# Performance work log

Measured on AMD Instinct MI355X. Metric: run time of the kernel, lower is better.

The kernel has to match this reference:

```python
import jax, jax.numpy as jnp
import numpy as np

HIDDEN = 256
N_PROT = 12288
N_MOL = 6144
N_BATCH = 32


def setup_inputs() -> dict:
    key = jax.random.key(0)
    ks = jax.random.split(key, 10)
    s = 1.0 / np.sqrt(HIDDEN)  # torch Linear default init scale
    inp = {
        "prot_embed": jax.random.normal(ks[0], (N_PROT, HIDDEN), jnp.float32),
        "mol_embed": jax.random.normal(ks[1], (N_MOL, HIDDEN), jnp.float32),
        "prot_batch": jnp.sort(jax.random.randint(ks[2], (N_PROT,), 0, N_BATCH)),
        "mol_batch": jnp.sort(jax.random.randint(ks[3], (N_MOL,), 0, N_BATCH)),
        "Wq": jax.random.uniform(ks[4], (HIDDEN, HIDDEN), jnp.float32, -s, s),
        "bq": jax.random.uniform(ks[5], (HIDDEN,), jnp.float32, -s, s),
        "Wk": jax.random.uniform(ks[6], (HIDDEN, HIDDEN), jnp.float32, -s, s),
        "bk": jax.random.uniform(ks[7], (HIDDEN,), jnp.float32, -s, s),
        "Wv": jax.random.uniform(ks[8], (HIDDEN, HIDDEN), jnp.float32, -s, s),
        "bv": jax.random.uniform(ks[9], (HIDDEN,), jnp.float32, -s, s),
    }
    return inp


def reference(prot_embed, mol_embed, prot_batch, mol_batch, Wq, bq, Wk, bk, Wv, bv):
    # Linear projections (torch nn.Linear: x @ W.T + b)
    Q = prot_embed @ Wq.T + bq            # [N, H]
    K = mol_embed @ Wk.T + bk             # [M, H]
    V = mol_embed @ Wv.T + bv             # [M, H]

    scale = 1.0 / jnp.sqrt(jnp.asarray(Q.shape[-1], Q.dtype))
    scores = (Q @ K.T) * scale            # [N, M]

    # block mask: same-batch pairs only
    mask = prot_batch[:, None] == mol_batch[None, :]   # [N, M] bool
    neg_inf = jnp.asarray(-jnp.inf, scores.dtype)
    scores = jnp.where(mask, scores, neg_inf)

    # stable masked softmax; rows with no valid key -> all zeros
    # (matches torch softmax(-inf row) -> nan -> nan_to_num(0.0))
    row_any = mask.any(axis=-1, keepdims=True)
    mx = jnp.max(scores, axis=-1, keepdims=True)
    mx = jnp.where(row_any, mx, 0.0)
    e = jnp.exp(scores - mx)              # exp(-inf)=0 on masked entries
    denom = jnp.sum(e, axis=-1, keepdims=True)
    attn = e / jnp.where(row_any, denom, 1.0)  # [N, M]

    out = attn @ V                        # [N, H]
    return out, attn
```

## Files before the change

### kernel.cpp

```cpp
#include <hip/hip_runtime.h>

#define NPROT 12288
#define NMOL  6144
#define HID   256
#define NB    32

#define WQ_O   4718592
#define WK_O   4784128
#define WV_O   4849664
#define BQ_O   4915200
#define BK_O   4915456
#define BV_O   4915712
#define Q_O    4915968
#define K_O    8061696
#define VT_O   9634560
#define END_O  11207424

typedef __attribute__((ext_vector_type(4))) float f32x4;
typedef __attribute__((ext_vector_type(8))) short bf16x8;
typedef unsigned short u16;
typedef unsigned int   u32;

__device__ __forceinline__ float b2f(u16 u){
  union { u32 i; float f; } v; v.i = ((u32)u) << 16; return v.f;
}
__device__ __forceinline__ u16 f2b(float f){
  union { float fl; u32 i; } v; v.fl = f;
  u32 i = v.i;
  return (u16)((i + 0x7FFFu + ((i >> 16) & 1u)) >> 16);
}

__global__ __launch_bounds__(256) void prep_kernel(
    const float* __restrict__ Wq, const float* __restrict__ Wk,
    const float* __restrict__ Wv, const float* __restrict__ bq,
    const float* __restrict__ bk, const float* __restrict__ bv,
    const int* __restrict__ pb, const int* __restrict__ mb,
    int* __restrict__ rg, u16* __restrict__ cvt)
{
  int g = blockIdx.x * 256 + threadIdx.x;
  const float* src = nullptr; u16* dst = nullptr; int off = 0;
  if      (g < 16384) { src = Wq; dst = cvt + WQ_O; off = g; }
  else if (g < 32768) { src = Wk; dst = cvt + WK_O; off = g - 16384; }
  else if (g < 49152) { src = Wv; dst = cvt + WV_O; off = g - 32768; }
  else if (g < 49216) { src = bq; dst = cvt + BQ_O; off = g - 49152; }
  else if (g < 49280) { src = bk; dst = cvt + BK_O; off = g - 49216; }
  else if (g < 49344) { src = bv; dst = cvt + BV_O; off = g - 49280; }
  if (src){
    f32x4 v = *(const f32x4*)(src + (size_t)off * 4);
    ushort4 o;
    o.x = f2b(v[0]); o.y = f2b(v[1]); o.z = f2b(v[2]); o.w = f2b(v[3]);
    *(ushort4*)(dst + (size_t)off * 4) = o;
  }

  if (blockIdx.x == 0 && threadIdx.x < 64){
    int t = threadIdx.x;
    const int* arr = (t < 32) ? pb : mb;
    int n          = (t < 32) ? NPROT : NMOL;
    int target     = (t & 31) + 1;
    int lo = 0, hi = n;
    while (lo < hi){
      int mid = (lo + hi) >> 1;
      if (arr[mid] < target) lo = mid + 1; else hi = mid;
    }
    int end = lo;
    int prev = __shfl(end, t - 1);
    int start = ((t & 31) == 0) ? 0 : prev;
    int b = t & 31;
    if (t < 32){ rg[b] = start; rg[32 + b] = end; }
    else       { rg[64 + b] = start; rg[96 + b] = end; }
  }
}

__global__ __launch_bounds__(256) void proj_kernel(
    const float* __restrict__ prot, const float* __restrict__ mol,
    const u16* __restrict__ cvt,
    u16* __restrict__ Q, u16* __restrict__ K, u16* __restrict__ Vt)
{
  __shared__ u16 xlds[16][264];
  __shared__ u16 tlds[4][64][18];
  int rb = blockIdx.x;
  int proj;
  const float* X; const u16 *W, *B;
  if      (rb < 768) { proj = 0; X = prot; W = cvt + WQ_O; B = cvt + BQ_O; }
  else if (rb < 1152){ proj = 1; rb -= 768;  X = mol; W = cvt + WK_O; B = cvt + BK_O; }
  else               { proj = 2; rb -= 1152; X = mol; W = cvt + WV_O; B = cvt + BV_O; }
  int rowbase = rb * 16;

  {
    int r  = threadIdx.x >> 4;
    int c0 = (threadIdx.x & 15) * 16;
    const float* xp = X + (size_t)(rowbase + r) * HID + c0;
    f32x4 v0 = *(const f32x4*)(xp);
    f32x4 v1 = *(const f32x4*)(xp + 4);
    f32x4 v2 = *(const f32x4*)(xp + 8);
    f32x4 v3 = *(const f32x4*)(xp + 12);
    u16* d = &xlds[r][c0];
    ushort4 o0, o1, o2, o3;
    o0.x = f2b(v0[0]); o0.y = f2b(v0[1]); o0.z = f2b(v0[2]); o0.w = f2b(v0[3]);
    o1.x = f2b(v1[0]); o1.y = f2b(v1[1]); o1.z = f2b(v1[2]); o1.w = f2b(v1[3]);
    o2.x = f2b(v2[0]); o2.y = f2b(v2[1]); o2.z = f2b(v2[2]); o2.w = f2b(v2[3]);
    o3.x = f2b(v3[0]); o3.y = f2b(v3[1]); o3.z = f2b(v3[2]); o3.w = f2b(v3[3]);
    *(ushort4*)(d)      = o0;
    *(ushort4*)(d + 4)  = o1;
    *(ushort4*)(d + 8)  = o2;
    *(ushort4*)(d + 12) = o3;
  }
  __syncthreads();

  int wave = threadIdx.x >> 6, lane = threadIdx.x & 63;
  int m = lane & 15, q = lane >> 4;
  int colbase = wave * 64;

  f32x4 acc[4] = {};
  for (int k0 = 0; k0 < HID; k0 += 32){
    bf16x8 a = *(const bf16x8*)(&xlds[m][k0 + q*8]);
    #pragma unroll
    for (int ct = 0; ct < 4; ct++){
      bf16x8 b = *(const bf16x8*)(W + (size_t)(colbase + ct*16 + m) * HID + k0 + q*8);
      acc[ct] = __builtin_amdgcn_mfma_f32_16x16x32_bf16(a, b, acc[ct], 0, 0, 0);
    }
  }

  if (proj < 2){
    u16* O = (proj == 0) ? Q : K;
    #pragma unroll
    for (int ct = 0; ct < 4; ct++){
      int col = colbase + ct*16 + m;
      float bb = b2f(B[col]);
      #pragma unroll
      for (int r = 0; r < 4; r++){
        int row = rowbase + q*4 + r;
        O[(size_t)row * HID + col] = f2b(acc[ct][r] + bb);
      }
    }
  } else {
    #pragma unroll
    for (int ct = 0; ct < 4; ct++){
      int lc = ct*16 + m;
      float bb = b2f(B[colbase + lc]);
      #pragma unroll
      for (int r = 0; r < 4; r++)
        tlds[wave][lc][q*4 + r] = f2b(acc[ct][r] + bb);
    }
    __syncthreads();
    int col = colbase + lane;
    u32 packed[8];
    #pragma unroll
    for (int i = 0; i < 8; i++){
      u16 lo = tlds[wave][lane][2*i];
      u16 hi = tlds[wave][lane][2*i+1];
      packed[i] = (u32)lo | ((u32)hi << 16);
    }
    u16* dst = Vt + (size_t)col * NMOL + rowbase;
    uint4 v0 = {packed[0], packed[1], packed[2], packed[3]};
    uint4 v1 = {packed[4], packed[5], packed[6], packed[7]};
    *(uint4*)dst = v0;
    *(uint4*)(dst + 8) = v1;
  }
}

__global__ __launch_bounds__(256) void attn_kernel(
    const int* __restrict__ rg,
    const u16* __restrict__ Q, const u16* __restrict__ K,
    const u16* __restrict__ Vt, float* __restrict__ dout)
{
  __shared__ u16 P[16][392];
  __shared__ float mxw[4][16];
  __shared__ float smw[4][16];
  const float scale = 0.0625f;
  float* outf  = dout;
  float* attnf = dout + (size_t)NPROT * HID;

  int b = blockIdx.y;
  int ps = rg[b], pe = rg[32+b], ms = rg[64+b], me = rg[96+b];
  int Np = pe - ps, Nm = me - ms;
  if (Np <= 0) return;

  int wave = threadIdx.x >> 6, lane = threadIdx.x & 63;
  int m = lane & 15, q = lane >> 4;
  int ntiles = (Np + 15) >> 4;

  int bs = 0, ce = 0;
  if (Nm > 0){ bs = ms & ~31; ce = bs + ((me - bs + 31) & ~31); }

  for (int tile = blockIdx.x; tile < ntiles; tile += 32){
    int row0 = ps + tile * 16;
    int qr = min(row0 + m, NPROT - 1);
    const u16* qrow = Q + (size_t)qr * HID;
    bf16x8 qf[8];
    #pragma unroll
    for (int kk = 0; kk < 8; kk++)
      qf[kk] = *(const bf16x8*)(qrow + kk*32 + q*8);

    if (Nm > 0){
      int myj0 = bs + wave * 16;
      f32x4 sreg[6];
      float mx[4] = {-1e30f, -1e30f, -1e30f, -1e30f};
      #pragma unroll
      for (int c = 0; c < 6; c++){
        int j0 = myj0 + 64*c;
        if (j0 < ce){
          int col = j0 + m;
          bool valid = (col >= ms) && (col < me);
          const u16* krow = K + (size_t)col * HID;
          f32x4 s0 = {0.f,0.f,0.f,0.f}, s1 = {0.f,0.f,0.f,0.f};
          #pragma unroll
          for (int kk = 0; kk < 4; kk++){
            bf16x8 kb0 = *(const bf16x8*)(krow + kk*32 + q*8);
            bf16x8 kb1 = *(const bf16x8*)(krow + (kk+4)*32 + q*8);
            s0 = __builtin_amdgcn_mfma_f32_16x16x32_bf16(qf[kk],   kb0, s0, 0, 0, 0);
            s1 = __builtin_amdgcn_mfma_f32_16x16x32_bf16(qf[kk+4], kb1, s1, 0, 0, 0);
          }
          f32x4 sv;
          #pragma unroll
          for (int r = 0; r < 4; r++)
            sv[r] = valid ? (s0[r] + s1[r]) * scale : -1e30f;
          sreg[c] = sv;
          float cm[4];
          #pragma unroll
          for (int r = 0; r < 4; r++) cm[r] = sv[r];
          #pragma unroll
          for (int d = 1; d < 16; d <<= 1)
            #pragma unroll
            for (int r = 0; r < 4; r++)
              cm[r] = fmaxf(cm[r], __shfl_xor(cm[r], d, 16));
          #pragma unroll
          for (int r = 0; r < 4; r++) mx[r] = fmaxf(mx[r], cm[r]);
        }
      }
      if (m == 0){
        #pragma unroll
        for (int r = 0; r < 4; r++) mxw[wave][q*4 + r] = mx[r];
      }
      __syncthreads();
      float gmx[4];
      #pragma unroll
      for (int r = 0; r < 4; r++){
        int row = q*4 + r;
        float M = mxw[0][row];
        #pragma unroll
        for (int w = 1; w < 4; w++) M = fmaxf(M, mxw[w][row]);
        gmx[r] = M;
      }

      float sm[4] = {0.f, 0.f, 0.f, 0.f};
      #pragma unroll
      for (int c = 0; c < 6; c++){
        int j0 = myj0 + 64*c;
        if (j0 < ce){
          f32x4 e;
          #pragma unroll
          for (int r = 0; r < 4; r++) e[r] = __expf(sreg[c][r] - gmx[r]);
          sreg[c] = e;
          float t[4];
          #pragma unroll
          for (int r = 0; r < 4; r++) t[r] = e[r];
          #pragma unroll
          for (int d = 1; d < 16; d <<= 1)
            #pragma unroll
            for (int r = 0; r < 4; r++)
              t[r] += __shfl_xor(t[r], d, 16);
          #pragma unroll
          for (int r = 0; r < 4; r++) sm[r] += t[r];
        }
      }
      if (m == 0){
        #pragma unroll
        for (int r = 0; r < 4; r++) smw[wave][q*4 + r] = sm[r];
      }
      __syncthreads();
      float ginv[4];
      #pragma unroll
      for (int r = 0; r < 4; r++){
        int row = q*4 + r;
        float S = smw[0][row] + smw[1][row] + smw[2][row] + smw[3][row];
        ginv[r] = (S > 0.f) ? (1.f / S) : 0.f;
      }

      #pragma unroll
      for (int c = 0; c < 6; c++){
        int j0 = myj0 + 64*c;
        if (j0 < ce){
          int col = j0 + m;
          int jl = j0 - bs;
          bool valid = (col >= ms) && (col < me);
          #pragma unroll
          for (int r = 0; r < 4; r++){
            float p = sreg[c][r] * ginv[r];
            P[q*4 + r][jl + m] = f2b(p);
            int row = row0 + q*4 + r;
            if (valid && row < pe)
              __builtin_nontemporal_store(p, attnf + (size_t)row * NMOL + col);
          }
        }
      }
      __syncthreads();

      f32x4 oacc[4] = {};
      for (int j0 = bs; j0 < ce; j0 += 32){
        int jl = j0 - bs;
        bf16x8 a = *(const bf16x8*)(&P[m][jl + q*8]);
        #pragma unroll
        for (int c2 = 0; c2 < 4; c2++){
          int ct = wave*4 + c2;
          bf16x8 vb = *(const bf16x8*)(Vt + (size_t)(ct*16 + m) * NMOL + j0 + q*8);
          oacc[c2] = __builtin_amdgcn_mfma_f32_16x16x32_bf16(a, vb, oacc[c2], 0, 0, 0);
        }
      }
      #pragma unroll
      for (int c2 = 0; c2 < 4; c2++){
        int col = (wave*4 + c2)*16 + m;
        #pragma unroll
        for (int r = 0; r < 4; r++){
          int row = row0 + q*4 + r;
          if (row < pe) outf[(size_t)row * HID + col] = oacc[c2][r];
        }
      }
    } else {
      #pragma unroll
      for (int c2 = 0; c2 < 4; c2++){
        int col = (wave*4 + c2)*16 + m;
        #pragma unroll
        for (int r = 0; r < 4; r++){
          int row = row0 + q*4 + r;
          if (row < pe) outf[(size_t)row * HID + col] = 0.f;
        }
      }
    }
    __syncthreads();
  }
}

extern "C" void kernel_launch(void* const* d_in, const int* in_sizes, int n_in,
                              void* d_out, int out_size, void* d_ws, size_t ws_size,
                              hipStream_t stream)
{
  (void)in_sizes; (void)n_in; (void)out_size;
  const float* prot = (const float*)d_in[0];
  const float* mol  = (const float*)d_in[1];
  const int* pb     = (const int*)d_in[2];
  const int* mb     = (const int*)d_in[3];
  const float* Wq   = (const float*)d_in[4];
  const float* bq   = (const float*)d_in[5];
  const float* Wk   = (const float*)d_in[6];
  const float* bk   = (const float*)d_in[7];
  const float* Wv   = (const float*)d_in[8];
  const float* bv   = (const float*)d_in[9];

  const size_t need = 1024 + (size_t)END_O * 2;
  if (ws_size < need) return;

  char* ws = (char*)d_ws;
  int* rg  = (int*)ws;
  u16* cvt = (u16*)(ws + 1024);
  u16* Qp  = cvt + Q_O;
  u16* Kp  = cvt + K_O;
  u16* Vtp = cvt + VT_O;
  float* out = (float*)d_out;

  prep_kernel<<<dim3(193), dim3(256), 0, stream>>>(
      Wq, Wk, Wv, bq, bk, bv, pb, mb, rg, cvt);
  proj_kernel<<<dim3(1536), dim3(256), 0, stream>>>(
      prot, mol, cvt, Qp, Kp, Vtp);
  attn_kernel<<<dim3(32, NB), dim3(256), 0, stream>>>(rg, Qp, Kp, Vtp, out);
}
```

Before: 354.0 us.

## Merge softmax max/sum barriers via online rescaling and double-buffer shared state

Replaces the separate cross-wave max reduction barrier with per-wave local max and sum, combined after a single barrier using online-softmax rescaling (exp of local minus global max). Shared P, max and sum buffers are double-buffered by tile parity so the trailing end-of-tile barrier can be dropped. This removes two of four block barriers per tile at the cost of extra exps and doubled shared memory, which may reduce occupancy. Local-max exponentials risk no overflow since each wave uses its own max.

```diff
diff --git a/kernel.cpp b/kernel.cpp
--- a/kernel.cpp
+++ b/kernel.cpp
@@ -164,9 +164,9 @@
     const u16* __restrict__ Q, const u16* __restrict__ K,
     const u16* __restrict__ Vt, float* __restrict__ dout)
 {
-  __shared__ u16 P[16][392];
-  __shared__ float mxw[4][16];
-  __shared__ float smw[4][16];
+  __shared__ u16 P[2][16][392];
+  __shared__ float mxw[2][4][16];
+  __shared__ float smw[2][4][16];
   const float scale = 0.0625f;
   float* outf  = dout;
   float* attnf = dout + (size_t)NPROT * HID;
@@ -183,6 +183,7 @@
   int bs = 0, ce = 0;
   if (Nm > 0){ bs = ms & ~31; ce = bs + ((me - bs + 31) & ~31); }
 
+  int pty = 0;
   for (int tile = blockIdx.x; tile < ntiles; tile += 32){
     int row0 = ps + tile * 16;
     int qr = min(row0 + m, NPROT - 1);
@@ -228,20 +229,6 @@
           for (int r = 0; r < 4; r++) mx[r] = fmaxf(mx[r], cm[r]);
         }
       }
-      if (m == 0){
-        #pragma unroll
-        for (int r = 0; r < 4; r++) mxw[wave][q*4 + r] = mx[r];
-      }
-      __syncthreads();
-      float gmx[4];
-      #pragma unroll
-      for (int r = 0; r < 4; r++){
-        int row = q*4 + r;
-        float M = mxw[0][row];
-        #pragma unroll
-        for (int w = 1; w < 4; w++) M = fmaxf(M, mxw[w][row]);
-        gmx[r] = M;
-      }
 
       float sm[4] = {0.f, 0.f, 0.f, 0.f};
       #pragma unroll
@@ -250,7 +237,7 @@
         if (j0 < ce){
           f32x4 e;
           #pragma unroll
-          for (int r = 0; r < 4; r++) e[r] = __expf(sreg[c][r] - gmx[r]);
+          for (int r = 0; r < 4; r++) e[r] = __expf(sreg[c][r] - mx[r]);
           sreg[c] = e;
           float t[4];
           #pragma unroll
@@ -266,15 +253,24 @@
       }
       if (m == 0){
         #pragma unroll
-        for (int r = 0; r < 4; r++) smw[wave][q*4 + r] = sm[r];
+        for (int r = 0; r < 4; r++){
+          mxw[pty][wave][q*4 + r] = mx[r];
+          smw[pty][wave][q*4 + r] = sm[r];
+        }
       }
       __syncthreads();
       float ginv[4];
       #pragma unroll
       for (int r = 0; r < 4; r++){
         int row = q*4 + r;
-        float S = smw[0][row] + smw[1][row] + smw[2][row] + smw[3][row];
-        ginv[r] = (S > 0.f) ? (1.f / S) : 0.f;
+        float M = mxw[pty][0][row];
+        #pragma unroll
+        for (int w = 1; w < 4; w++) M = fmaxf(M, mxw[pty][w][row]);
+        float L = 0.f;
+        #pragma unroll
+        for (int w = 0; w < 4; w++)
+          L += smw[pty][w][row] * __expf(mxw[pty][w][row] - M);
+        ginv[r] = (L > 0.f) ? (__expf(mx[r] - M) / L) : 0.f;
       }
 
       #pragma unroll
@@ -287,7 +283,7 @@
           #pragma unroll
           for (int r = 0; r < 4; r++){
             float p = sreg[c][r] * ginv[r];
-            P[q*4 + r][jl + m] = f2b(p);
+            P[pty][q*4 + r][jl + m] = f2b(p);
             int row = row0 + q*4 + r;
             if (valid && row < pe)
               __builtin_nontemporal_store(p, attnf + (size_t)row * NMOL + col);
@@ -299,7 +295,7 @@
       f32x4 oacc[4] = {};
       for (int j0 = bs; j0 < ce; j0 += 32){
         int jl = j0 - bs;
-        bf16x8 a = *(const bf16x8*)(&P[m][jl + q*8]);
+        bf16x8 a = *(const bf16x8*)(&P[pty][m][jl + q*8]);
         #pragma unroll
         for (int c2 = 0; c2 < 4; c2++){
           int ct = wave*4 + c2;
@@ -327,7 +323,7 @@
         }
       }
     }
-    __syncthreads();
+    pty ^= 1;
   }
 }
 
```

Result: no change. 353.5 us (-0.1%).
